# Kernel tuning notes

Hardware: AMD Instinct MI355X
Metric: run time of the kernel (lower is better)

## Reference

```python
import jax, jax.numpy as jnp
import numpy as np

EMBED = 1024
HEADS = 16
HEAD_DIM = EMBED // HEADS
SEQ = 2048
BATCH = 2


def setup_inputs() -> dict:
    key = jax.random.key(0)
    ks = jax.random.split(key, 5)
    s = 1.0 / np.sqrt(EMBED)
    return {
        "x": jax.random.normal(ks[0], (BATCH, SEQ, EMBED), jnp.float32),
        "W_qkv": jax.random.uniform(ks[1], (EMBED, 3 * EMBED), jnp.float32, -s, s),
        "b_qkv": jax.random.uniform(ks[2], (3 * EMBED,), jnp.float32, -s, s),
        "W_out": jax.random.uniform(ks[3], (EMBED, EMBED), jnp.float32, -s, s),
        "b_out": jax.random.uniform(ks[4], (EMBED,), jnp.float32, -s, s),
    }


def reference(x, W_qkv, b_qkv, W_out, b_out):
    B, S, E = x.shape
    qkv = x @ W_qkv + b_qkv                      # [B,S,3E]
    q, k, v = jnp.split(qkv, 3, axis=-1)
    # [B,S,E] -> [B,H,S,D]
    def heads(t):
        return t.reshape(B, S, HEADS, HEAD_DIM).transpose(0, 2, 1, 3)
    q, k, v = heads(q), heads(k), heads(v)
    scores = jnp.einsum("bhid,bhjd->bhij", q, k) / np.sqrt(HEAD_DIM)  # [B,H,S,S]
    causal = jnp.tril(jnp.ones((S, S), bool))
    scores = jnp.where(causal[None, None], scores, -jnp.inf)
    probs = jax.nn.softmax(scores, axis=-1)
    out = jnp.einsum("bhij,bhjd->bhid", probs, v)  # [B,H,S,D]
    out = out.transpose(0, 2, 1, 3).reshape(B, S, E)
    return out @ W_out + b_out
```

## Files before the change

### kernel.cpp

```cpp
#include <hip/hip_runtime.h>
#include <hip/hip_bf16.h>
#include <cstdint>
#include <cstddef>


typedef unsigned short u16;
typedef __attribute__((ext_vector_type(8))) short short8;
typedef __attribute__((ext_vector_type(4))) short short4v;
typedef __attribute__((ext_vector_type(4))) float floatx4;

#define MFMA16(a, b, c) __builtin_amdgcn_mfma_f32_16x16x32_bf16((a), (b), (c), 0, 0, 0)

#if __has_builtin(__builtin_amdgcn_mfma_f32_16x16x16_bf16)
#define PV_MFMA(a, b, c) __builtin_amdgcn_mfma_f32_16x16x16_bf16((a), (b), (c), 0, 0, 0)
#elif __has_builtin(__builtin_amdgcn_mfma_f32_16x16x16bf16_1k)
#define PV_MFMA(a, b, c) __builtin_amdgcn_mfma_f32_16x16x16bf16_1k((a), (b), (c), 0, 0, 0)
#else
static __device__ __forceinline__ floatx4 pv_mfma_asm(short4v a, short4v b, floatx4 c) {
    asm volatile("v_mfma_f32_16x16x16_bf16 %0, %1, %2, %0" : "+v"(c) : "v"(a), "v"(b));
    return c;
}
#define PV_MFMA(a, b, c) pv_mfma_asm((a), (b), (c))
#endif

#if __has_builtin(__builtin_amdgcn_exp2f)
#define EXP2(x) __builtin_amdgcn_exp2f(x)
#else
#define EXP2(x) exp2f(x)
#endif

#define QSCALE 0.18033688011f
#define NEGINF (-__builtin_inff())
#define DEFER_THR 8.0f

static __device__ __forceinline__ u16 f2b(float f) {
    union { float f; uint32_t u; } v; v.f = f;
    return (u16)((v.u + 0x7fffu + ((v.u >> 16) & 1u)) >> 16);
}

static __device__ __forceinline__ uint32_t pkbf(float lo, float hi) {
    union { float f; uint32_t u; } a, b; a.f = lo; b.f = hi;
    return __builtin_amdgcn_perm(b.u + 0x8000u, a.u + 0x8000u, 0x07060302u);
}

static __device__ __forceinline__ void async_cp16(const u16* g, u16* lds_wave_base) {
    __builtin_amdgcn_global_load_lds((__attribute__((address_space(1))) void*)g,
                                     (__attribute__((address_space(3))) void*)lds_wave_base,
                                     16, 0, 0);
}


__global__ __launch_bounds__(256) void k_prep(const float* __restrict__ x,
                                              const float* __restrict__ Wq,
                                              const float* __restrict__ Wo,
                                              u16* __restrict__ xb,
                                              u16* __restrict__ wqkvT,
                                              u16* __restrict__ woutT) {
    int bx = blockIdx.x, tid = threadIdx.x;
    if (bx < 2048) {
        int g = bx * 256 + tid;
        const float4* s = (const float4*)x + (size_t)g * 2;
        float4 f0 = s[0], f1 = s[1];
        uint4 r;
        r.x = pkbf(f0.x, f0.y);
        r.y = pkbf(f0.z, f0.w);
        r.z = pkbf(f1.x, f1.y);
        r.w = pkbf(f1.z, f1.w);
        *(uint4*)(xb + (size_t)g * 8) = r;
        return;
    }
    __shared__ float t[32][33];
    const float* src;
    u16* dst;
    int R, C, b;
    if (bx < 5120) { b = bx - 2048; src = Wq; dst = wqkvT; R = 1024; C = 3072; }
    else           { b = bx - 5120; src = Wo; dst = woutT; R = 1024; C = 1024; }
    int nbx = C >> 5;
    int yq = b / nbx, xq = b - yq * nbx;
    int c0 = xq * 32, r0 = yq * 32;
    int tx = tid & 31, ty = tid >> 5;
#pragma unroll
    for (int i = 0; i < 4; ++i)
        t[ty + i * 8][tx] = src[(size_t)(r0 + ty + i * 8) * C + c0 + tx];
    __syncthreads();
#pragma unroll
    for (int i = 0; i < 4; ++i)
        dst[(size_t)(c0 + ty + i * 8) * R + r0 + tx] = f2b(t[tx][ty + i * 8]);
}


__global__ __launch_bounds__(256, 3) void k_qkv_gemm(const u16* __restrict__ A,
                                                     const u16* __restrict__ Bt,
                                                     const float* __restrict__ bias,
                                                     u16* __restrict__ Qb,
                                                     u16* __restrict__ Kb,
                                                     u16* __restrict__ Vtb) {
    __shared__ __align__(16) u16 As[3][128 * 32];
    __shared__ __align__(16) u16 Bs[3][128 * 32];
    int tid = threadIdx.x;
    int w = tid >> 6, lane = tid & 63, quad = lane >> 4, l16 = lane & 15;
    int wm = w >> 1, wn = w & 1;
    int m0 = blockIdx.y * 128, n0 = blockIdx.x * 128;
    int wb = (tid & ~63) * 8;

    int ra0 = tid >> 2, ca0 = (tid & 3) * 8;
    int ra1 = (256 + tid) >> 2, ca1 = (tid & 3) * 8;
    const u16* A0 = &A[(size_t)(m0 + ra0) * 1024 + ca0];
    const u16* A1 = &A[(size_t)(m0 + ra1) * 1024 + ca1];
    const u16* B0 = &Bt[(size_t)(n0 + ra0) * 1024 + ca0];
    const u16* B1 = &Bt[(size_t)(n0 + ra1) * 1024 + ca1];

    auto stage = [&](int src_kt, int slot) {
        int ko = src_kt * 32;
        async_cp16(A0 + ko, &As[slot][wb]);
        async_cp16(A1 + ko, &As[slot][2048 + wb]);
        async_cp16(B0 + ko, &Bs[slot][wb]);
        async_cp16(B1 + ko, &Bs[slot][2048 + wb]);
    };

    floatx4 acc[4][4] = {};
    stage(0, 0);
    stage(1, 1);

    for (int kt = 0; kt < 32; ++kt) {
        asm volatile("s_waitcnt vmcnt(4)" ::: "memory");
        asm volatile("s_barrier" ::: "memory");
        int jn = kt + 2;
        stage(jn < 32 ? jn : 31, jn % 3);
        int s = kt % 3;
        short8 af[4], bf[4];
#pragma unroll
        for (int mt = 0; mt < 4; ++mt)
            af[mt] = *(const short8*)&As[s][(wm * 64 + mt * 16 + l16) * 32 + quad * 8];
#pragma unroll
        for (int nt = 0; nt < 4; ++nt)
            bf[nt] = *(const short8*)&Bs[s][(wn * 64 + nt * 16 + l16) * 32 + quad * 8];
#pragma unroll
        for (int mt = 0; mt < 4; ++mt)
#pragma unroll
            for (int nt = 0; nt < 4; ++nt)
                acc[mt][nt] = MFMA16(af[mt], bf[nt], acc[mt][nt]);
    }

    int region = n0 >> 10;
    if (region == 2) {
#pragma unroll
        for (int mt = 0; mt < 4; ++mt)
#pragma unroll
            for (int nt = 0; nt < 4; ++nt) {
                int n_abs = n0 + wn * 64 + nt * 16 + l16;
                int e = n_abs & 1023, h = e >> 6, d = e & 63;
                float vb = bias[n_abs];
                int mrow = m0 + wm * 64 + mt * 16 + quad * 4;
                int b = mrow >> 11, s0 = mrow & 2047;
                uint2 val;
                val.x = pkbf(acc[mt][nt][0] + vb, acc[mt][nt][1] + vb);
                val.y = pkbf(acc[mt][nt][2] + vb, acc[mt][nt][3] + vb);
                *(uint2*)&Vtb[((size_t)(b * 16 + h) * 64 + d) * 2048 + s0] = val;
            }
    } else {
        u16* dst = region == 0 ? Qb : Kb;
        float scl = region == 0 ? QSCALE : 1.0f;
#pragma unroll
        for (int mt = 0; mt < 4; ++mt)
#pragma unroll
            for (int nt = 0; nt < 4; ++nt)
#pragma unroll
                for (int r = 0; r < 4; ++r) {
                    int m_abs = m0 + wm * 64 + mt * 16 + quad * 4 + r;
                    int n_abs = n0 + wn * 64 + nt * 16 + l16;
                    float val = (acc[mt][nt][r] + bias[n_abs]) * scl;
                    int e = n_abs & 1023, h = e >> 6, d = e & 63;
                    int b = m_abs >> 11, s = m_abs & 2047;
                    dst[((size_t)(b * 16 + h) * 2048 + s) * 64 + d] = f2b(val);
                }
    }
}


__global__ __launch_bounds__(256, 4) void k_out_gemm(const u16* __restrict__ A,
                                                     const u16* __restrict__ Bt,
                                                     const float* __restrict__ bias,
                                                     float* __restrict__ out) {
    __shared__ __align__(16) u16 As[3][64 * 32];
    __shared__ __align__(16) u16 Bs[3][128 * 32];
    int tid = threadIdx.x;
    int w = tid >> 6, lane = tid & 63, quad = lane >> 4, l16 = lane & 15;
    int wm = w >> 1, wn = w & 1;
    int m0 = blockIdx.y * 64, n0 = blockIdx.x * 128;
    int wb = (tid & ~63) * 8;

    int ra0 = tid >> 2, ca0 = (tid & 3) * 8;
    int ra1 = (256 + tid) >> 2;
    const u16* A0 = &A[(size_t)(m0 + ra0) * 1024 + ca0];
    const u16* B0 = &Bt[(size_t)(n0 + ra0) * 1024 + ca0];
    const u16* B1 = &Bt[(size_t)(n0 + ra1) * 1024 + ca0];

    auto stage = [&](int src_kt, int slot) {
        int ko = src_kt * 32;
        async_cp16(A0 + ko, &As[slot][wb]);
        async_cp16(B0 + ko, &Bs[slot][wb]);
        async_cp16(B1 + ko, &Bs[slot][2048 + wb]);
    };

    floatx4 acc[2][4] = {};
    stage(0, 0);
    stage(1, 1);

    for (int kt = 0; kt < 32; ++kt) {
        asm volatile("s_waitcnt vmcnt(3)" ::: "memory");
        asm volatile("s_barrier" ::: "memory");
        int jn = kt + 2;
        stage(jn < 32 ? jn : 31, jn % 3);
        int s = kt % 3;
        short8 af[2], bf[4];
#pragma unroll
        for (int mt = 0; mt < 2; ++mt)
            af[mt] = *(const short8*)&As[s][(wm * 32 + mt * 16 + l16) * 32 + quad * 8];
#pragma unroll
        for (int nt = 0; nt < 4; ++nt)
            bf[nt] = *(const short8*)&Bs[s][(wn * 64 + nt * 16 + l16) * 32 + quad * 8];
#pragma unroll
        for (int mt = 0; mt < 2; ++mt)
#pragma unroll
            for (int nt = 0; nt < 4; ++nt)
                acc[mt][nt] = MFMA16(af[mt], bf[nt], acc[mt][nt]);
    }

#pragma unroll
    for (int mt = 0; mt < 2; ++mt)
#pragma unroll
        for (int nt = 0; nt < 4; ++nt)
#pragma unroll
            for (int r = 0; r < 4; ++r) {
                int m_abs = m0 + wm * 32 + mt * 16 + quad * 4 + r;
                int n_abs = n0 + wn * 64 + nt * 16 + l16;
                out[(size_t)m_abs * 1024 + n_abs] = acc[mt][nt][r] + bias[n_abs];
            }
}


__global__ __launch_bounds__(256, 2) void k_attn(const u16* __restrict__ Qb,
                                                 const u16* __restrict__ Kb,
                                                 const u16* __restrict__ Vtb,
                                                 u16* __restrict__ attnb) {
    __shared__ __align__(16) u16 KV[4][2][4096];
    int tid = threadIdx.x;
    int w = tid >> 6, lane = tid & 63, quad = lane >> 4, l16 = lane & 15;
    int L = blockIdx.x;
    int bh = ((L & 7) << 2) | ((L >> 3) & 3);
    int idx = (L >> 5) & 15;
    int tile = idx < 8 ? idx : 23 - idx;
    const u16* Qp = Qb + (size_t)bh * 131072;
    const u16* Kp = Kb + (size_t)bh * 131072;
    const u16* Vp = Vtb + (size_t)bh * 131072;
    int b = bh >> 4, h = bh & 15;

    int r0 = tid >> 3, c0 = ((tid & 7) ^ (r0 & 7)) * 8;
    int f1 = 256 + tid;
    int r1 = f1 >> 3, c1 = ((f1 & 7) ^ (r1 & 7)) * 8;
    int kOff0 = r0 * 64 + c0, kOff1 = r1 * 64 + c1;
    int vOff0 = r0 * 2048 + c0, vOff1 = r1 * 2048 + c1;
    int wb = (tid & ~63) * 8;

    int q_s0 = tile * 128 + w * 16 + l16;
    int q_s1 = q_s0 + 64;
    short8 q00 = *(const short8*)&Qp[(size_t)q_s0 * 64 + quad * 8];
    short8 q01 = *(const short8*)&Qp[(size_t)q_s0 * 64 + 32 + quad * 8];
    short8 q10 = *(const short8*)&Qp[(size_t)q_s1 * 64 + quad * 8];
    short8 q11 = *(const short8*)&Qp[(size_t)q_s1 * 64 + 32 + quad * 8];

    int n = 2 * tile + 2;

    auto stage = [&](int j) {
        u16* Ks = (u16*)KV[j & 3][0];
        u16* Vs = (u16*)KV[j & 3][1];
        const u16* kp = Kp + (size_t)j * 4096;
        const u16* vp = Vp + (size_t)j * 64;
        async_cp16(kp + kOff0, Ks + wb);
        async_cp16(kp + kOff1, Ks + 2048 + wb);
        async_cp16(vp + vOff0, Vs + wb);
        async_cp16(vp + vOff1, Vs + 2048 + wb);
    };

    floatx4 acc0[4] = {}, acc1[4] = {};
    float m0 = NEGINF, l0 = 0.f;
    float m1 = NEGINF, l1 = 0.f;
    int sw = l16 & 7;

    stage(0); stage(1); stage(2);

    for (int kt = 0; kt < n; ++kt) {
        asm volatile("s_waitcnt vmcnt(8)" ::: "memory");
        asm volatile("s_barrier" ::: "memory");
        {
            int jn = kt + 3;
            stage(jn < n ? jn : n - 1);
        }
        const u16* Ks = (const u16*)KV[kt & 3][0];
        const u16* Vs = (const u16*)KV[kt & 3][1];

        short8 kfa[4], kfb[4];
#pragma unroll
        for (int nt = 0; nt < 4; ++nt) {
            int rb = (nt * 16 + l16) * 8;
            kfa[nt] = *(const short8*)&Ks[(rb + (quad ^ sw)) * 8];
            kfb[nt] = *(const short8*)&Ks[(rb + ((4 + quad) ^ sw)) * 8];
        }
        short4v vf[4][4];
#pragma unroll
        for (int dt = 0; dt < 4; ++dt) {
            const char* rowb = (const char*)Vs + (dt * 16 + l16) * 128 + (quad & 1) * 8;
#pragma unroll
            for (int nt = 0; nt < 4; ++nt) {
                int chunk = nt * 2 + (quad >> 1);
                vf[nt][dt] = *(const short4v*)(rowb + ((chunk ^ sw) * 16));
            }
        }

        auto tile_step = [&](short8 qf0, short8 qf1, int q_abs, bool diag, float& mr,
                             float& lp, floatx4* accO) {
            floatx4 sa[4] = {};
#pragma unroll
            for (int nt = 0; nt < 4; ++nt) {
                sa[nt] = MFMA16(kfa[nt], qf0, sa[nt]);
                sa[nt] = MFMA16(kfb[nt], qf1, sa[nt]);
            }
            if (diag) {
#pragma unroll
                for (int nt = 0; nt < 4; ++nt)
#pragma unroll
                    for (int r = 0; r < 4; ++r)
                        if (kt * 64 + nt * 16 + quad * 4 + r > q_abs)
                            sa[nt][r] = NEGINF;
            }
            float t0 = fmaxf(fmaxf(sa[0][0], sa[0][1]), sa[0][2]);
            float t1 = fmaxf(fmaxf(sa[0][3], sa[1][0]), sa[1][1]);
            float t2 = fmaxf(fmaxf(sa[1][2], sa[1][3]), sa[2][0]);
            float t3 = fmaxf(fmaxf(sa[2][1], sa[2][2]), sa[2][3]);
            float t4 = fmaxf(fmaxf(sa[3][0], sa[3][1]), sa[3][2]);
            float v = fmaxf(fmaxf(fmaxf(t0, t1), t2),
                            fmaxf(fmaxf(t3, t4), sa[3][3]));
            if (!__all(v <= mr + DEFER_THR)) {
                float vr = fmaxf(v, __shfl_xor(v, 16));
                vr = fmaxf(vr, __shfl_xor(vr, 32));
                float m_new = fmaxf(mr, vr);
                float alpha = EXP2(mr - m_new);
                lp *= alpha;
#pragma unroll
                for (int dt = 0; dt < 4; ++dt)
#pragma unroll
                    for (int r = 0; r < 4; ++r) accO[dt][r] *= alpha;
                mr = m_new;
            }
            float p[4][4];
#pragma unroll
            for (int nt = 0; nt < 4; ++nt)
#pragma unroll
                for (int r = 0; r < 4; ++r)
                    p[nt][r] = EXP2(sa[nt][r] - mr);
            float s0 = (p[0][0] + p[0][1]) + (p[0][2] + p[0][3]);
            float s1 = (p[1][0] + p[1][1]) + (p[1][2] + p[1][3]);
            float s2 = (p[2][0] + p[2][1]) + (p[2][2] + p[2][3]);
            float s3 = (p[3][0] + p[3][1]) + (p[3][2] + p[3][3]);
            lp += (s0 + s1) + (s2 + s3);
#pragma unroll
            for (int nt = 0; nt < 4; ++nt) {
                union { uint2 u; short4v s; } pf;
                pf.u.x = pkbf(p[nt][0], p[nt][1]);
                pf.u.y = pkbf(p[nt][2], p[nt][3]);
#pragma unroll
                for (int dt = 0; dt < 4; ++dt)
                    accO[dt] = PV_MFMA(vf[nt][dt], pf.s, accO[dt]);
            }
        };

        tile_step(q10, q11, q_s1, kt == n - 1, m1, l1, acc1);
        if (kt < n - 1)
            tile_step(q00, q01, q_s0, kt == n - 2, m0, l0, acc0);
    }

    auto epilogue = [&](int q_abs, float lp, const floatx4* accO) {
        float lr = lp;
        lr += __shfl_xor(lr, 16);
        lr += __shfl_xor(lr, 32);
        float inv = 1.f / lr;
        size_t base = ((size_t)(b * 2048 + q_abs)) * 1024 + h * 64;
#pragma unroll
        for (int dt = 0; dt < 4; ++dt) {
            uint2 val;
            val.x = pkbf(accO[dt][0] * inv, accO[dt][1] * inv);
            val.y = pkbf(accO[dt][2] * inv, accO[dt][3] * inv);
            *(uint2*)&attnb[base + dt * 16 + quad * 4] = val;
        }
    };
    epilogue(q_s0, l0, acc0);
    epilogue(q_s1, l1, acc1);
}


extern "C" void kernel_launch(void* const* d_in, const int* in_sizes, int n_in,
                              void* d_out, int out_size, void* d_ws, size_t ws_size,
                              hipStream_t stream) {
    const float* x     = (const float*)d_in[0];
    const float* W_qkv = (const float*)d_in[1];
    const float* b_qkv = (const float*)d_in[2];
    const float* W_out = (const float*)d_in[3];
    const float* b_out = (const float*)d_in[4];
    float* out = (float*)d_out;

    char* p = (char*)d_ws;
    u16* xb    = (u16*)p; p += (size_t)4096 * 1024 * 2;
    u16* wqkvT = (u16*)p; p += (size_t)3072 * 1024 * 2;
    u16* woutT = (u16*)p; p += (size_t)1024 * 1024 * 2;
    u16* Qb    = (u16*)p; p += (size_t)32 * 2048 * 64 * 2;
    u16* Kb    = (u16*)p; p += (size_t)32 * 2048 * 64 * 2;
    u16* Vtb   = (u16*)p; p += (size_t)32 * 64 * 2048 * 2;
    u16* attnb = xb;

    k_prep<<<6144, 256, 0, stream>>>(x, W_qkv, W_out, xb, wqkvT, woutT);
    k_qkv_gemm<<<dim3(24, 32), 256, 0, stream>>>(xb, wqkvT, b_qkv, Qb, Kb, Vtb);
    k_attn<<<512, 256, 0, stream>>>(Qb, Kb, Vtb, attnb);
    k_out_gemm<<<dim3(8, 64), 256, 0, stream>>>(attnb, woutT, b_out, out);
}
```

Before: 175.1 us.

## Split attention query strips across 8 waves instead of 2 strips per wave

The attention kernel now launches 512 threads per block. Each of the 8 waves owns one 16-row query slice from one of the two 64-row strips, where before 4 waves each processed both strips serially. Each thread issues one async K/V copy per stage instead of two, and the wait count drops accordingly. This doubles the waves that share each staged K/V tile, which should raise occupancy and parallelism and cut per-wave register pressure. In exchange, the waves on the first strip sit idle through the final diagonal tile, and each extra wave re-reads K/V fragments from LDS.

```diff
diff --git a/kernel.cpp b/kernel.cpp
--- a/kernel.cpp
+++ b/kernel.cpp
@@ -240,7 +240,7 @@
 }
 
 
-__global__ __launch_bounds__(256, 2) void k_attn(const u16* __restrict__ Qb,
+__global__ __launch_bounds__(512, 4) void k_attn(const u16* __restrict__ Qb,
                                                  const u16* __restrict__ Kb,
                                                  const u16* __restrict__ Vtb,
                                                  u16* __restrict__ attnb) {
@@ -257,81 +257,72 @@
     int b = bh >> 4, h = bh & 15;
 
     int r0 = tid >> 3, c0 = ((tid & 7) ^ (r0 & 7)) * 8;
-    int f1 = 256 + tid;
-    int r1 = f1 >> 3, c1 = ((f1 & 7) ^ (r1 & 7)) * 8;
-    int kOff0 = r0 * 64 + c0, kOff1 = r1 * 64 + c1;
-    int vOff0 = r0 * 2048 + c0, vOff1 = r1 * 2048 + c1;
+    int kOff = r0 * 64 + c0;
+    int vOff = r0 * 2048 + c0;
     int wb = (tid & ~63) * 8;
 
-    int q_s0 = tile * 128 + w * 16 + l16;
-    int q_s1 = q_s0 + 64;
-    short8 q00 = *(const short8*)&Qp[(size_t)q_s0 * 64 + quad * 8];
-    short8 q01 = *(const short8*)&Qp[(size_t)q_s0 * 64 + 32 + quad * 8];
-    short8 q10 = *(const short8*)&Qp[(size_t)q_s1 * 64 + quad * 8];
-    short8 q11 = *(const short8*)&Qp[(size_t)q_s1 * 64 + 32 + quad * 8];
+    int strip = w >> 2;
+    int q_s = tile * 128 + strip * 64 + (w & 3) * 16 + l16;
+    short8 q0 = *(const short8*)&Qp[(size_t)q_s * 64 + quad * 8];
+    short8 q1 = *(const short8*)&Qp[(size_t)q_s * 64 + 32 + quad * 8];
 
     int n = 2 * tile + 2;
+    int lastk = n - 2 + strip;
 
     auto stage = [&](int j) {
         u16* Ks = (u16*)KV[j & 3][0];
         u16* Vs = (u16*)KV[j & 3][1];
-        const u16* kp = Kp + (size_t)j * 4096;
-        const u16* vp = Vp + (size_t)j * 64;
-        async_cp16(kp + kOff0, Ks + wb);
-        async_cp16(kp + kOff1, Ks + 2048 + wb);
-        async_cp16(vp + vOff0, Vs + wb);
-        async_cp16(vp + vOff1, Vs + 2048 + wb);
+        async_cp16(Kp + (size_t)j * 4096 + kOff, Ks + wb);
+        async_cp16(Vp + (size_t)j * 64 + vOff, Vs + wb);
     };
 
-    floatx4 acc0[4] = {}, acc1[4] = {};
-    float m0 = NEGINF, l0 = 0.f;
-    float m1 = NEGINF, l1 = 0.f;
+    floatx4 acc[4] = {};
+    float mr = NEGINF, lp = 0.f;
     int sw = l16 & 7;
 
     stage(0); stage(1); stage(2);
 
     for (int kt = 0; kt < n; ++kt) {
-        asm volatile("s_waitcnt vmcnt(8)" ::: "memory");
+        asm volatile("s_waitcnt vmcnt(4)" ::: "memory");
         asm volatile("s_barrier" ::: "memory");
         {
             int jn = kt + 3;
             stage(jn < n ? jn : n - 1);
         }
-        const u16* Ks = (const u16*)KV[kt & 3][0];
-        const u16* Vs = (const u16*)KV[kt & 3][1];
-
-        short8 kfa[4], kfb[4];
-#pragma unroll
-        for (int nt = 0; nt < 4; ++nt) {
-            int rb = (nt * 16 + l16) * 8;
-            kfa[nt] = *(const short8*)&Ks[(rb + (quad ^ sw)) * 8];
-            kfb[nt] = *(const short8*)&Ks[(rb + ((4 + quad) ^ sw)) * 8];
-        }
-        short4v vf[4][4];
-#pragma unroll
-        for (int dt = 0; dt < 4; ++dt) {
-            const char* rowb = (const char*)Vs + (dt * 16 + l16) * 128 + (quad & 1) * 8;
+        if (kt <= lastk) {
+            const u16* Ks = (const u16*)KV[kt & 3][0];
+            const u16* Vs = (const u16*)KV[kt & 3][1];
+
+            short8 kfa[4], kfb[4];
 #pragma unroll
             for (int nt = 0; nt < 4; ++nt) {
-                int chunk = nt * 2 + (quad >> 1);
-                vf[nt][dt] = *(const short4v*)(rowb + ((chunk ^ sw) * 16));
-            }
-        }
-
-        auto tile_step = [&](short8 qf0, short8 qf1, int q_abs, bool diag, float& mr,
-                             float& lp, floatx4* accO) {
+                int rb = (nt * 16 + l16) * 8;
+                kfa[nt] = *(const short8*)&Ks[(rb + (quad ^ sw)) * 8];
+                kfb[nt] = *(const short8*)&Ks[(rb + ((4 + quad) ^ sw)) * 8];
+            }
+            short4v vf[4][4];
+#pragma unroll
+            for (int dt = 0; dt < 4; ++dt) {
+                const char* rowb = (const char*)Vs + (dt * 16 + l16) * 128 + (quad & 1) * 8;
+#pragma unroll
+                for (int nt = 0; nt < 4; ++nt) {
+                    int chunk = nt * 2 + (quad >> 1);
+                    vf[nt][dt] = *(const short4v*)(rowb + ((chunk ^ sw) * 16));
+                }
+            }
+
             floatx4 sa[4] = {};
 #pragma unroll
             for (int nt = 0; nt < 4; ++nt) {
-                sa[nt] = MFMA16(kfa[nt], qf0, sa[nt]);
-                sa[nt] = MFMA16(kfb[nt], qf1, sa[nt]);
-            }
-            if (diag) {
+                sa[nt] = MFMA16(kfa[nt], q0, sa[nt]);
+                sa[nt] = MFMA16(kfb[nt], q1, sa[nt]);
+            }
+            if (kt == lastk) {
 #pragma unroll
                 for (int nt = 0; nt < 4; ++nt)
 #pragma unroll
                     for (int r = 0; r < 4; ++r)
-                        if (kt * 64 + nt * 16 + quad * 4 + r > q_abs)
+                        if (kt * 64 + nt * 16 + quad * 4 + r > q_s)
                             sa[nt][r] = NEGINF;
             }
             float t0 = fmaxf(fmaxf(sa[0][0], sa[0][1]), sa[0][2]);
@@ -350,7 +341,7 @@
 #pragma unroll
                 for (int dt = 0; dt < 4; ++dt)
 #pragma unroll
-                    for (int r = 0; r < 4; ++r) accO[dt][r] *= alpha;
+                    for (int r = 0; r < 4; ++r) acc[dt][r] *= alpha;
                 mr = m_new;
             }
             float p[4][4];
@@ -371,31 +362,23 @@
                 pf.u.y = pkbf(p[nt][2], p[nt][3]);
 #pragma unroll
                 for (int dt = 0; dt < 4; ++dt)
-                    accO[dt] = PV_MFMA(vf[nt][dt], pf.s, accO[dt]);
-            }
-        };
-
-        tile_step(q10, q11, q_s1, kt == n - 1, m1, l1, acc1);
-        if (kt < n - 1)
-            tile_step(q00, q01, q_s0, kt == n - 2, m0, l0, acc0);
-    }
-
-    auto epilogue = [&](int q_abs, float lp, const floatx4* accO) {
-        float lr = lp;
-        lr += __shfl_xor(lr, 16);
-        lr += __shfl_xor(lr, 32);
-        float inv = 1.f / lr;
-        size_t base = ((size_t)(b * 2048 + q_abs)) * 1024 + h * 64;
-#pragma unroll
-        for (int dt = 0; dt < 4; ++dt) {
-            uint2 val;
-            val.x = pkbf(accO[dt][0] * inv, accO[dt][1] * inv);
-            val.y = pkbf(accO[dt][2] * inv, accO[dt][3] * inv);
-            *(uint2*)&attnb[base + dt * 16 + quad * 4] = val;
+                    acc[dt] = PV_MFMA(vf[nt][dt], pf.s, acc[dt]);
+            }
         }
-    };
-    epilogue(q_s0, l0, acc0);
-    epilogue(q_s1, l1, acc1);
+    }
+
+    float lr = lp;
+    lr += __shfl_xor(lr, 16);
+    lr += __shfl_xor(lr, 32);
+    float inv = 1.f / lr;
+    size_t base = ((size_t)(b * 2048 + q_s)) * 1024 + h * 64;
+#pragma unroll
+    for (int dt = 0; dt < 4; ++dt) {
+        uint2 val;
+        val.x = pkbf(acc[dt][0] * inv, acc[dt][1] * inv);
+        val.y = pkbf(acc[dt][2] * inv, acc[dt][3] * inv);
+        *(uint2*)&attnb[base + dt * 16 + quad * 4] = val;
+    }
 }
 
 
@@ -420,6 +403,6 @@
 
     k_prep<<<6144, 256, 0, stream>>>(x, W_qkv, W_out, xb, wqkvT, woutT);
     k_qkv_gemm<<<dim3(24, 32), 256, 0, stream>>>(xb, wqkvT, b_qkv, Qb, Kb, Vtb);
-    k_attn<<<512, 256, 0, stream>>>(Qb, Kb, Vtb, attnb);
+    k_attn<<<512, 512, 0, stream>>>(Qb, Kb, Vtb, attnb);
     k_out_gemm<<<dim3(8, 64), 256, 0, stream>>>(attnb, woutT, b_out, out);
 }
```

Measured after the change: 174.3 us. No clear change (-0.4%).
